# Optimization experiments

Hardware: AMD Instinct MI355X
Metric: run time of the kernel (lower is better)

## Reference

```python
import jax, jax.numpy as jnp
import numpy as np


def _area2d(a, b, c):
    # signed parallelogram area; broadcasts (b may be a [S,S,2] grid)
    return (b[..., 0] - a[..., 0]) * (c[..., 1] - a[..., 1]) - (b[..., 1] - a[..., 1]) * (c[..., 0] - a[..., 0])


def _lookup_table(size):
    # matches torch: meshgrid(ij) of linspace(-1,1), stack [xx,yy], rot90
    lin = jnp.linspace(-1.0, 1.0, size, dtype=jnp.float32)
    xx, yy = jnp.meshgrid(lin, lin, indexing='ij')
    t = jnp.stack([xx, yy], axis=-1)
    return jnp.rot90(t, 1)  # [S,S,2] screen-space (x,y) per pixel


def _grid_sample(img, grid):
    # bilinear, zeros padding, align_corners=True (old 4-arg ATen grid_sampler_2d)
    C, H, W = img.shape
    x = (grid[..., 0] + 1.0) * 0.5 * (W - 1)
    y = (grid[..., 1] + 1.0) * 0.5 * (H - 1)
    x0 = jnp.floor(x)
    y0 = jnp.floor(y)
    wx = x - x0
    wy = y - y0

    def gather(ix, iy):
        inb = (ix >= 0) & (ix <= W - 1) & (iy >= 0) & (iy <= H - 1)
        ii = jnp.clip(ix, 0, W - 1).astype(jnp.int32)
        jj = jnp.clip(iy, 0, H - 1).astype(jnp.int32)
        return img[:, jj, ii] * inb[None].astype(img.dtype)  # [C,h,w]

    v00 = gather(x0, y0)
    v10 = gather(x0 + 1, y0)
    v01 = gather(x0, y0 + 1)
    v11 = gather(x0 + 1, y0 + 1)
    return (v00 * ((1 - wx) * (1 - wy))[None] + v10 * (wx * (1 - wy))[None]
            + v01 * ((1 - wx) * wy)[None] + v11 * (wx * wy)[None])


def _render(tris, uvs, uvmap, size):
    S = size
    pts = _lookup_table(S)            # [S,S,2]
    uvs_v = uvs * 2.0 - 1.0           # module maps uvs from [0,1] to [-1,1]
    zmin = jnp.min(tris.reshape(-1, 3), axis=0)[2]
    zbuf0 = jnp.full((S, S), zmin, dtype=tris.dtype)
    res0 = jnp.zeros((4, S, S), dtype=tris.dtype)

    def step(carry, tu):
        zbuf, res = carry
        tri, uv = tu                  # tri [3,3], uv [3,2]
        t2 = tri[:, :2]
        w = _area2d(t2[0], t2[1], t2[2])
        valid = w >= 1e-9             # degenerate triangle -> skipped (masked out)
        ws = jnp.where(valid, w, 1.0)
        pAB = _area2d(t2[1], pts, t2[0])
        pCB = _area2d(t2[2], pts, t2[1])
        pCA = _area2d(t2[0], pts, t2[2])
        inside = (jnp.maximum(pAB, 0.0) * jnp.maximum(pCB, 0.0) * jnp.maximum(pCA, 0.0) > 0) & valid
        w1 = pCB / ws
        w2 = pCA / ws
        w3 = 1.0 - w1 - w2
        pts3d = w1[..., None] * tri[0] + w2[..., None] * tri[1] + w3[..., None] * tri[2]  # [S,S,3]
        z = pts3d[..., 2]
        zmsk = z >= zbuf
        ptsUV = w1[..., None] * uv[0] + w2[..., None] * uv[1] + w3[..., None] * uv[2]      # [S,S,2]
        rgb = _grid_sample(uvmap, ptsUV)[:3]  # [3,S,S]
        rmsk = inside & zmsk
        zbuf = jnp.where(rmsk, z, zbuf)
        res = jnp.concatenate([jnp.where(rmsk[None], rgb, res[:3]),
                               jnp.where(rmsk, 1.0, res[3])[None]], axis=0)
        return (zbuf, res), None

    (_, res), _ = jax.lax.scan(step, (zbuf0, res0), (tris, uvs_v))
    return res


def setup_inputs():
    key = jax.random.key(0)
    k1, k2, k3 = jax.random.split(key, 3)
    tris = jax.random.uniform(k1, (256, 3, 3), jnp.float32, -1.0, 1.0)
    uvs = jax.random.uniform(k2, (256, 3, 2), jnp.float32)
    uvmap = jax.random.uniform(k3, (3, 1024, 1024), jnp.float32)
    return {"tris": tris, "uvs": uvs, "uvmap": uvmap, "size": 256}


def reference(tris, uvs, uvmap, size):
    return _render(tris, uvs, uvmap, size)
```

## Files before the change

kernel.cpp:

```cpp
#include <hip/hip_runtime.h>


#define S 256
#define TMAX 256
#define NC 4
#define BT 1024

__global__ __launch_bounds__(BT) void render_kernel(
    const float* __restrict__ tris,
    const float* __restrict__ uvs,
    const float* __restrict__ uvmap,
    float* __restrict__ out,
    int T)
{
#pragma clang fp contract(off)
    __shared__ float4 sd[TMAX][6];
    __shared__ float  zred[BT];
    __shared__ float4 cand[NC][S];

    const int tid = threadIdx.x;

    float zl = 3.0e38f;
    for (int t = tid; t < T; t += BT) {
        const float* p = tris + t * 9;
        float Ax = p[0], Ay = p[1], Az = p[2];
        float Bx = p[3], By = p[4], Bz = p[5];
        float Cx = p[6], Cy = p[7], Cz = p[8];
        float w = (Bx - Ax) * (Cy - Ay) - (By - Ay) * (Cx - Ax);
        bool valid = (w >= 1e-9f);
        const float* q = uvs + t * 6;
        sd[t][0] = make_float4(Bx, By, Ay - By, Ax - Bx);
        sd[t][1] = make_float4(Cx, Cy, By - Cy, Bx - Cx);
        sd[t][2] = make_float4(Ax, Ay, Cy - Ay, Cx - Ax);
        sd[t][3] = make_float4(valid ? w : 1.0f, Az, Bz, Cz);
        sd[t][4] = make_float4(valid ? 1.0f : 0.0f,
                               q[0] * 2.0f - 1.0f, q[1] * 2.0f - 1.0f, q[2] * 2.0f - 1.0f);
        sd[t][5] = make_float4(q[3] * 2.0f - 1.0f, q[4] * 2.0f - 1.0f, q[5] * 2.0f - 1.0f, 0.0f);
        zl = fminf(zl, fminf(Az, fminf(Bz, Cz)));
    }
    zred[tid] = zl;
    __syncthreads();
    for (int s = BT / 2; s > 0; s >>= 1) {
        if (tid < s) zred[tid] = fminf(zred[tid], zred[tid + s]);
        __syncthreads();
    }
    const float zmin = zred[0];

    const int i = blockIdx.x;
    const int c = tid >> 8;
    const int j = tid & (S - 1);
    const float px = (float)(-1.0 + (double)j * (2.0 / 255.0));
    const float py = (float)(-1.0 + (double)(S - 1 - i) * (2.0 / 255.0));

    const int cs   = (T + NC - 1) / NC;
    const int tbeg = c * cs;
    const int tend = (tbeg + cs < T) ? (tbeg + cs) : T;

    float zcur = zmin;
    int win = -1;
    float w1w = 0.0f, w2w = 0.0f;

    for (int t = tbeg; t < tend; ++t) {
        float4 r0 = sd[t][0];
        float4 r1 = sd[t][1];
        float4 r2 = sd[t][2];
        float4 r3 = sd[t][3];
        float vld = sd[t][4].x;
        float pAB = (px - r0.x) * r0.z - (py - r0.y) * r0.w;
        float pCB = (px - r1.x) * r1.z - (py - r1.y) * r1.w;
        float pCA = (px - r2.x) * r2.z - (py - r2.y) * r2.w;
        float prod = fmaxf(pAB, 0.0f) * fmaxf(pCB, 0.0f) * fmaxf(pCA, 0.0f);
        bool inside = (prod > 0.0f) && (vld != 0.0f);
        if (inside) {
            float w1 = pCB / r3.x;
            float w2 = pCA / r3.x;
            float w3 = (1.0f - w1) - w2;
            float z = (w1 * r3.y + w2 * r3.z) + w3 * r3.w;
            if (z >= zcur) { zcur = z; win = t; w1w = w1; w2w = w2; }
        }
    }
    cand[c][j] = make_float4(zcur, w1w, w2w, (float)win);
    __syncthreads();

    if (tid < S) {
        float zb = 0.0f, w1 = 0.0f, w2 = 0.0f;
        int w = -1;
        #pragma unroll
        for (int k = 0; k < NC; ++k) {
            float4 ck = cand[k][tid];
            int cw = (int)ck.w;
            if (cw >= 0 && (w < 0 || ck.x >= zb)) {
                zb = ck.x; w1 = ck.y; w2 = ck.z; w = cw;
            }
        }

        float r = 0.0f, g = 0.0f, b = 0.0f, a = 0.0f;
        if (w >= 0) {
            a = 1.0f;
            float w3 = (1.0f - w1) - w2;
            float4 r4 = sd[w][4];
            float4 r5 = sd[w][5];
            float ux = (w1 * r4.y + w2 * r4.w) + w3 * r5.y;
            float uy = (w1 * r4.z + w2 * r5.x) + w3 * r5.z;
            float X = ((ux + 1.0f) * 0.5f) * 1023.0f;
            float Y = ((uy + 1.0f) * 0.5f) * 1023.0f;
            float x0 = floorf(X), y0 = floorf(Y);
            float wx = X - x0, wy = Y - y0;
            float w00 = (1.0f - wx) * (1.0f - wy);
            float w10 = wx * (1.0f - wy);
            float w01 = (1.0f - wx) * wy;
            float w11 = wx * wy;
            float xs1 = x0 + 1.0f, ys1 = y0 + 1.0f;
            bool xin0 = (x0  >= 0.0f) && (x0  <= 1023.0f);
            bool xin1 = (xs1 >= 0.0f) && (xs1 <= 1023.0f);
            bool yin0 = (y0  >= 0.0f) && (y0  <= 1023.0f);
            bool yin1 = (ys1 >= 0.0f) && (ys1 <= 1023.0f);
            int xi0 = (int)fminf(fmaxf(x0,  0.0f), 1023.0f);
            int xi1 = (int)fminf(fmaxf(xs1, 0.0f), 1023.0f);
            int yi0 = (int)fminf(fmaxf(y0,  0.0f), 1023.0f);
            int yi1 = (int)fminf(fmaxf(ys1, 0.0f), 1023.0f);
            float acc[3];
            #pragma unroll
            for (int ch = 0; ch < 3; ++ch) {
                const float* img = uvmap + ch * (1024 * 1024);
                float v00 = (xin0 && yin0) ? img[yi0 * 1024 + xi0] : 0.0f;
                float v10 = (xin1 && yin0) ? img[yi0 * 1024 + xi1] : 0.0f;
                float v01 = (xin0 && yin1) ? img[yi1 * 1024 + xi0] : 0.0f;
                float v11 = (xin1 && yin1) ? img[yi1 * 1024 + xi1] : 0.0f;
                acc[ch] = ((v00 * w00 + v10 * w10) + v01 * w01) + v11 * w11;
            }
            r = acc[0]; g = acc[1]; b = acc[2];
        }

        const int base = i * S + tid;
        out[0 * S * S + base] = r;
        out[1 * S * S + base] = g;
        out[2 * S * S + base] = b;
        out[3 * S * S + base] = a;
    }
}

extern "C" void kernel_launch(void* const* d_in, const int* in_sizes, int n_in,
                              void* d_out, int out_size, void* d_ws, size_t ws_size,
                              hipStream_t stream) {
    const float* tris  = (const float*)d_in[0];
    const float* uvs   = (const float*)d_in[1];
    const float* uvmap = (const float*)d_in[2];
    float* out = (float*)d_out;
    int T = in_sizes[0] / 9;
    if (T > TMAX) T = TMAX;
    render_kernel<<<dim3(S), dim3(BT), 0, stream>>>(tris, uvs, uvmap, out, T);
}
```

Measured before the change: 89.02 us.

## Precompute triangle records in a prep kernel and read them via scalar loads

Moves per-triangle setup and the global z-min reduction out of the render kernel into a single-block prep kernel. That kernel writes the records to workspace memory. Each of the 256 render blocks then stops redoing the setup, the 1024-wide LDS reduction and its barriers. The render loop reads records from global memory with a wave-uniform index (via readfirstlane), so the loads can go through the scalar path instead of LDS. Degenerate triangles get zeroed edge terms, which removes the validity check from the inner loop. The cost is an extra kernel launch and a global-memory dependency between the two kernels.

```diff
diff --git a/kernel.cpp b/kernel.cpp
--- a/kernel.cpp
+++ b/kernel.cpp
@@ -5,23 +5,19 @@
 #define TMAX 256
 #define NC 4
 #define BT 1024
+#define RECF 24
 
-__global__ __launch_bounds__(BT) void render_kernel(
+__global__ __launch_bounds__(256) void prep_kernel(
     const float* __restrict__ tris,
     const float* __restrict__ uvs,
-    const float* __restrict__ uvmap,
-    float* __restrict__ out,
+    float* __restrict__ rec,
     int T)
 {
 #pragma clang fp contract(off)
-    __shared__ float4 sd[TMAX][6];
-    __shared__ float  zred[BT];
-    __shared__ float4 cand[NC][S];
-
-    const int tid = threadIdx.x;
-
+    __shared__ float zred[256];
+    const int t = threadIdx.x;
     float zl = 3.0e38f;
-    for (int t = tid; t < T; t += BT) {
+    if (t < T) {
         const float* p = tris + t * 9;
         float Ax = p[0], Ay = p[1], Az = p[2];
         float Bx = p[3], By = p[4], Bz = p[5];
@@ -29,26 +25,47 @@
         float w = (Bx - Ax) * (Cy - Ay) - (By - Ay) * (Cx - Ax);
         bool valid = (w >= 1e-9f);
         const float* q = uvs + t * 6;
-        sd[t][0] = make_float4(Bx, By, Ay - By, Ax - Bx);
-        sd[t][1] = make_float4(Cx, Cy, By - Cy, Bx - Cx);
-        sd[t][2] = make_float4(Ax, Ay, Cy - Ay, Cx - Ax);
-        sd[t][3] = make_float4(valid ? w : 1.0f, Az, Bz, Cz);
-        sd[t][4] = make_float4(valid ? 1.0f : 0.0f,
-                               q[0] * 2.0f - 1.0f, q[1] * 2.0f - 1.0f, q[2] * 2.0f - 1.0f);
-        sd[t][5] = make_float4(q[3] * 2.0f - 1.0f, q[4] * 2.0f - 1.0f, q[5] * 2.0f - 1.0f, 0.0f);
+        float4* r = (float4*)(rec + t * RECF);
+        if (valid) {
+            r[0] = make_float4(Bx, By, Ay - By, Ax - Bx);
+            r[1] = make_float4(Cx, Cy, By - Cy, Bx - Cx);
+            r[2] = make_float4(Ax, Ay, Cy - Ay, Cx - Ax);
+        } else {
+            r[0] = make_float4(0.f, 0.f, 0.f, 0.f);
+            r[1] = make_float4(0.f, 0.f, 0.f, 0.f);
+            r[2] = make_float4(0.f, 0.f, 0.f, 0.f);
+        }
+        r[3] = make_float4(valid ? w : 1.0f, Az, Bz, Cz);
+        r[4] = make_float4(q[0] * 2.0f - 1.0f, q[1] * 2.0f - 1.0f,
+                           q[2] * 2.0f - 1.0f, q[3] * 2.0f - 1.0f);
+        r[5] = make_float4(q[4] * 2.0f - 1.0f, q[5] * 2.0f - 1.0f, 0.f, 0.f);
         zl = fminf(zl, fminf(Az, fminf(Bz, Cz)));
     }
-    zred[tid] = zl;
+    zred[t] = zl;
     __syncthreads();
-    for (int s = BT / 2; s > 0; s >>= 1) {
-        if (tid < s) zred[tid] = fminf(zred[tid], zred[tid + s]);
+    for (int s = 128; s > 0; s >>= 1) {
+        if (t < s) zred[t] = fminf(zred[t], zred[t + s]);
         __syncthreads();
     }
-    const float zmin = zred[0];
+    if (t == 0) rec[TMAX * RECF] = zred[0];
+}
 
+__global__ __launch_bounds__(BT) void render_kernel(
+    const float* __restrict__ rec,
+    const float* __restrict__ uvmap,
+    float* __restrict__ out,
+    int T)
+{
+#pragma clang fp contract(off)
+    __shared__ float4 cand[NC][S];
+
+    const int tid = threadIdx.x;
     const int i = blockIdx.x;
-    const int c = tid >> 8;
+    const int c = __builtin_amdgcn_readfirstlane(tid >> 8);
     const int j = tid & (S - 1);
+
+    const float zmin = rec[TMAX * RECF];
+
     const float px = (float)(-1.0 + (double)j * (2.0 / 255.0));
     const float py = (float)(-1.0 + (double)(S - 1 - i) * (2.0 / 255.0));
 
@@ -61,17 +78,16 @@
     float w1w = 0.0f, w2w = 0.0f;
 
     for (int t = tbeg; t < tend; ++t) {
-        float4 r0 = sd[t][0];
-        float4 r1 = sd[t][1];
-        float4 r2 = sd[t][2];
-        float4 r3 = sd[t][3];
-        float vld = sd[t][4].x;
+        const float4* r = (const float4*)(rec + t * RECF);
+        float4 r0 = r[0];
+        float4 r1 = r[1];
+        float4 r2 = r[2];
+        float4 r3 = r[3];
         float pAB = (px - r0.x) * r0.z - (py - r0.y) * r0.w;
         float pCB = (px - r1.x) * r1.z - (py - r1.y) * r1.w;
         float pCA = (px - r2.x) * r2.z - (py - r2.y) * r2.w;
         float prod = fmaxf(pAB, 0.0f) * fmaxf(pCB, 0.0f) * fmaxf(pCA, 0.0f);
-        bool inside = (prod > 0.0f) && (vld != 0.0f);
-        if (inside) {
+        if (prod > 0.0f) {
             float w1 = pCB / r3.x;
             float w2 = pCA / r3.x;
             float w3 = (1.0f - w1) - w2;
@@ -98,10 +114,11 @@
         if (w >= 0) {
             a = 1.0f;
             float w3 = (1.0f - w1) - w2;
-            float4 r4 = sd[w][4];
-            float4 r5 = sd[w][5];
-            float ux = (w1 * r4.y + w2 * r4.w) + w3 * r5.y;
-            float uy = (w1 * r4.z + w2 * r5.x) + w3 * r5.z;
+            const float4* rw = (const float4*)(rec + w * RECF);
+            float4 r4 = rw[4];
+            float4 r5 = rw[5];
+            float ux = (w1 * r4.x + w2 * r4.z) + w3 * r5.x;
+            float uy = (w1 * r4.y + w2 * r4.w) + w3 * r5.y;
             float X = ((ux + 1.0f) * 0.5f) * 1023.0f;
             float Y = ((uy + 1.0f) * 0.5f) * 1023.0f;
             float x0 = floorf(X), y0 = floorf(Y);
@@ -147,7 +164,9 @@
     const float* uvs   = (const float*)d_in[1];
     const float* uvmap = (const float*)d_in[2];
     float* out = (float*)d_out;
+    float* rec = (float*)d_ws;
     int T = in_sizes[0] / 9;
     if (T > TMAX) T = TMAX;
-    render_kernel<<<dim3(S), dim3(BT), 0, stream>>>(tris, uvs, uvmap, out, T);
+    prep_kernel<<<dim3(1), dim3(256), 0, stream>>>(tris, uvs, rec, T);
+    render_kernel<<<dim3(S), dim3(BT), 0, stream>>>(rec, uvmap, out, T);
 }
```

Measured after the change: 97.21 us. 1.09x slower.

## Cull triangles per row by y-extent and split rows across two blocks

Applied to the files above, without the earlier changes.

Each block now covers half a row, which doubles the grid, and splits the triangle list eight ways instead of four. Before rasterizing, it builds a compacted list of valid triangles whose y-range (plus a small margin) contains the row, using ballot and popcount. Per-pixel edge tests then run only over this culled list. UV data is read from global memory only for the winning triangle, and the z-min reduction is shrunk to 256 entries. The cost is that the per-block setup and culling is repeated in twice as many blocks, and the margin has to be wide enough that no edge pixel is wrongly excluded.

```diff
diff --git a/kernel.cpp b/kernel.cpp
--- a/kernel.cpp
+++ b/kernel.cpp
@@ -3,8 +3,10 @@
 
 #define S 256
 #define TMAX 256
-#define NC 4
+#define NC 8
 #define BT 1024
+#define HALF 128
+#define MARGIN 0.02f
 
 __global__ __launch_bounds__(BT) void render_kernel(
     const float* __restrict__ tris,
@@ -14,75 +16,99 @@
     int T)
 {
 #pragma clang fp contract(off)
-    __shared__ float4 sd[TMAX][6];
-    __shared__ float  zred[BT];
-    __shared__ float4 cand[NC][S];
+    __shared__ float4 sd[TMAX][4];
+    __shared__ float  zred[TMAX];
+    __shared__ int    list[TMAX];
+    __shared__ unsigned long long masks[4];
+    __shared__ int    woff[5];
+    __shared__ float4 cand[NC][HALF];
 
-    const int tid = threadIdx.x;
+    const int tid  = threadIdx.x;
+    const int bid  = blockIdx.x;
+    const int row  = bid >> 1;
+    const int half = bid & 1;
+    const int j    = half * HALF + (tid & (HALF - 1));
+    const int c    = tid >> 7;
 
-    float zl = 3.0e38f;
-    for (int t = tid; t < T; t += BT) {
-        const float* p = tris + t * 9;
-        float Ax = p[0], Ay = p[1], Az = p[2];
-        float Bx = p[3], By = p[4], Bz = p[5];
-        float Cx = p[6], Cy = p[7], Cz = p[8];
-        float w = (Bx - Ax) * (Cy - Ay) - (By - Ay) * (Cx - Ax);
-        bool valid = (w >= 1e-9f);
-        const float* q = uvs + t * 6;
-        sd[t][0] = make_float4(Bx, By, Ay - By, Ax - Bx);
-        sd[t][1] = make_float4(Cx, Cy, By - Cy, Bx - Cx);
-        sd[t][2] = make_float4(Ax, Ay, Cy - Ay, Cx - Ax);
-        sd[t][3] = make_float4(valid ? w : 1.0f, Az, Bz, Cz);
-        sd[t][4] = make_float4(valid ? 1.0f : 0.0f,
-                               q[0] * 2.0f - 1.0f, q[1] * 2.0f - 1.0f, q[2] * 2.0f - 1.0f);
-        sd[t][5] = make_float4(q[3] * 2.0f - 1.0f, q[4] * 2.0f - 1.0f, q[5] * 2.0f - 1.0f, 0.0f);
-        zl = fminf(zl, fminf(Az, fminf(Bz, Cz)));
+    const float px = (float)(-1.0 + (double)j * (2.0 / 255.0));
+    const float py = (float)(-1.0 + (double)(S - 1 - row) * (2.0 / 255.0));
+
+    bool keep = false;
+    if (tid < TMAX) {
+        if (tid < T) {
+            const float* p = tris + tid * 9;
+            float Ax = p[0], Ay = p[1], Az = p[2];
+            float Bx = p[3], By = p[4], Bz = p[5];
+            float Cx = p[6], Cy = p[7], Cz = p[8];
+            float w = (Bx - Ax) * (Cy - Ay) - (By - Ay) * (Cx - Ax);
+            bool valid = (w >= 1e-9f);
+            sd[tid][0] = make_float4(Bx, By, Ay - By, Ax - Bx);
+            sd[tid][1] = make_float4(Cx, Cy, By - Cy, Bx - Cx);
+            sd[tid][2] = make_float4(Ax, Ay, Cy - Ay, Cx - Ax);
+            sd[tid][3] = make_float4(valid ? w : 1.0f, Az, Bz, Cz);
+            zred[tid] = fminf(Az, fminf(Bz, Cz));
+            float ymn = fminf(Ay, fminf(By, Cy));
+            float ymx = fmaxf(Ay, fmaxf(By, Cy));
+            keep = valid && (py >= ymn - MARGIN) && (py <= ymx + MARGIN);
+        } else {
+            zred[tid] = 3.0e38f;
+        }
     }
-    zred[tid] = zl;
+    unsigned long long m = __ballot(keep);
+    if (tid < TMAX && (tid & 63) == 0) masks[tid >> 6] = m;
     __syncthreads();
-    for (int s = BT / 2; s > 0; s >>= 1) {
+
+    if (tid == 512) {
+        int s = 0;
+        #pragma unroll
+        for (int k = 0; k < 4; ++k) { woff[k] = s; s += __popcll(masks[k]); }
+        woff[4] = s;
+    }
+    for (int s = TMAX / 2; s > 0; s >>= 1) {
         if (tid < s) zred[tid] = fminf(zred[tid], zred[tid + s]);
         __syncthreads();
     }
-    const float zmin = zred[0];
+    if (tid < TMAX && keep) {
+        int lane = tid & 63;
+        int wv   = tid >> 6;
+        int pos  = woff[wv] + __popcll(masks[wv] & ((1ull << lane) - 1ull));
+        list[pos] = tid;
+    }
+    __syncthreads();
 
-    const int i = blockIdx.x;
-    const int c = tid >> 8;
-    const int j = tid & (S - 1);
-    const float px = (float)(-1.0 + (double)j * (2.0 / 255.0));
-    const float py = (float)(-1.0 + (double)(S - 1 - i) * (2.0 / 255.0));
+    const float zmin  = zred[0];
+    const int   nlive = woff[4];
 
-    const int cs   = (T + NC - 1) / NC;
-    const int tbeg = c * cs;
-    const int tend = (tbeg + cs < T) ? (tbeg + cs) : T;
+    const int cs = (nlive + NC - 1) / NC;
+    const int tb = c * cs;
+    const int te = (tb + cs < nlive) ? (tb + cs) : nlive;
 
     float zcur = zmin;
     int win = -1;
     float w1w = 0.0f, w2w = 0.0f;
 
-    for (int t = tbeg; t < tend; ++t) {
-        float4 r0 = sd[t][0];
-        float4 r1 = sd[t][1];
-        float4 r2 = sd[t][2];
-        float4 r3 = sd[t][3];
-        float vld = sd[t][4].x;
+    for (int it = tb; it < te; ++it) {
+        int tt = list[it];
+        float4 r0 = sd[tt][0];
+        float4 r1 = sd[tt][1];
+        float4 r2 = sd[tt][2];
+        float4 r3 = sd[tt][3];
         float pAB = (px - r0.x) * r0.z - (py - r0.y) * r0.w;
         float pCB = (px - r1.x) * r1.z - (py - r1.y) * r1.w;
         float pCA = (px - r2.x) * r2.z - (py - r2.y) * r2.w;
         float prod = fmaxf(pAB, 0.0f) * fmaxf(pCB, 0.0f) * fmaxf(pCA, 0.0f);
-        bool inside = (prod > 0.0f) && (vld != 0.0f);
-        if (inside) {
+        if (prod > 0.0f) {
             float w1 = pCB / r3.x;
             float w2 = pCA / r3.x;
             float w3 = (1.0f - w1) - w2;
             float z = (w1 * r3.y + w2 * r3.z) + w3 * r3.w;
-            if (z >= zcur) { zcur = z; win = t; w1w = w1; w2w = w2; }
+            if (z >= zcur) { zcur = z; win = tt; w1w = w1; w2w = w2; }
         }
     }
-    cand[c][j] = make_float4(zcur, w1w, w2w, (float)win);
+    cand[c][tid & (HALF - 1)] = make_float4(zcur, w1w, w2w, (float)win);
     __syncthreads();
 
-    if (tid < S) {
+    if (tid < HALF) {
         float zb = 0.0f, w1 = 0.0f, w2 = 0.0f;
         int w = -1;
         #pragma unroll
@@ -98,10 +124,12 @@
         if (w >= 0) {
             a = 1.0f;
             float w3 = (1.0f - w1) - w2;
-            float4 r4 = sd[w][4];
-            float4 r5 = sd[w][5];
-            float ux = (w1 * r4.y + w2 * r4.w) + w3 * r5.y;
-            float uy = (w1 * r4.z + w2 * r5.x) + w3 * r5.z;
+            const float* q = uvs + w * 6;
+            float u0x = q[0] * 2.0f - 1.0f, u0y = q[1] * 2.0f - 1.0f;
+            float u1x = q[2] * 2.0f - 1.0f, u1y = q[3] * 2.0f - 1.0f;
+            float u2x = q[4] * 2.0f - 1.0f, u2y = q[5] * 2.0f - 1.0f;
+            float ux = (w1 * u0x + w2 * u1x) + w3 * u2x;
+            float uy = (w1 * u0y + w2 * u1y) + w3 * u2y;
             float X = ((ux + 1.0f) * 0.5f) * 1023.0f;
             float Y = ((uy + 1.0f) * 0.5f) * 1023.0f;
             float x0 = floorf(X), y0 = floorf(Y);
@@ -132,7 +160,7 @@
             r = acc[0]; g = acc[1]; b = acc[2];
         }
 
-        const int base = i * S + tid;
+        const int base = row * S + j;
         out[0 * S * S + base] = r;
         out[1 * S * S + base] = g;
         out[2 * S * S + base] = b;
@@ -149,5 +177,5 @@
     float* out = (float*)d_out;
     int T = in_sizes[0] / 9;
     if (T > TMAX) T = TMAX;
-    render_kernel<<<dim3(S), dim3(BT), 0, stream>>>(tris, uvs, uvmap, out, T);
+    render_kernel<<<dim3(2 * S), dim3(BT), 0, stream>>>(tris, uvs, uvmap, out, T);
 }
```

Result: faster. 78.27 us (-12.1%).
